# Kernel optimization log

Hardware: AMD Instinct MI355X
Metric: run time of the kernel (lower is better)

The kernel has to match this reference:

```python
import jax, jax.numpy as jnp
import numpy as np

LAMDA = 0.2  # config['lamda']
T, B, NI, IL, NS, H = 24, 64, 32, 24, 256, 256  # steps, batch, n_inputs, input_len(=vec), n_stations, hidden


def setup_inputs() -> dict:
    key = jax.random.key(0)
    ks = jax.random.split(key, 24)
    VEC, DIN = IL, NI + NS
    n = lambda k, s, sc=1.0: jax.random.normal(k, s, dtype=jnp.float32) * sc
    return {
        'local_inputs': n(ks[0], (T, B, NI)),
        'global_inputs': n(ks[1], (T, B, NS)),
        'local_states': n(ks[2], (B, NI, IL)),
        'global_states': n(ks[3], (B, NS, NI, IL)),
        'distmat': n(ks[4], (B, NS)),
        'local_attn0': jax.random.uniform(ks[5], (B, NI), jnp.float32, -0.25, 0.25),
        'global_attn0': jax.random.uniform(ks[6], (B, NS), jnp.float32, -0.15, 0.15),
        # conv_local_u: 1x1 conv over [B, IL, NI, 1] -> weight [VEC, IL]
        'Wcl': n(ks[7], (VEC, IL), 0.1), 'bcl': n(ks[8], (VEC,), 0.05),
        'Wll': n(ks[9], (VEC, H), 0.05), 'bll': n(ks[10], (VEC,), 0.05),
        'vl': n(ks[11], (VEC,)),
        # conv_global_k: kernel (1, NI) over [B, IL, NS, NI] -> weight [VEC, IL, NI]
        'Wcg': n(ks[12], (VEC, IL, NI), 0.05), 'bcg': n(ks[13], (VEC,), 0.05),
        'Wlg': n(ks[14], (VEC, H), 0.05), 'blg': n(ks[15], (VEC,), 0.05),
        'vg': n(ks[16], (VEC,)),
        # LSTM cell (called with zero h0/c0 every step, as in the source)
        'Wih': n(ks[17], (4 * H, DIN), 0.05),
        'bih': n(ks[18], (4 * H,), 0.05),
        'bhh': n(ks[19], (4 * H,), 0.05),
    }


def reference(local_inputs, global_inputs, local_states, global_states, distmat,
              local_attn0, global_attn0, Wcl, bcl, Wll, bll, vl,
              Wcg, bcg, Wlg, blg, vg, Wih, bih, bhh):
    b, ni, il = local_states.shape
    ns = global_states.shape[1]
    # raw .view() reshapes as in the torch code (NOT transposes)
    lhid = local_states.reshape(b, il, ni)                 # [B, IL, NI]
    hf_l = jnp.einsum('oc,bcl->bol', Wcl, lhid) + bcl[None, :, None]   # 1x1 conv
    ghid = global_states.reshape(b, il, ns, ni)            # [B, IL, NS, NI]
    hf_g = jnp.einsum('ocj,bcsj->bos', Wcg, ghid) + bcg[None, :, None]  # (1,NI) conv

    def step(carry, xs):
        la, ga = carry
        l_inp, g_inp = xs
        x = jnp.concatenate([la * l_inp, ga * g_inp], axis=1)  # [B, NI+NS]
        gates = x @ Wih.T + bih + bhh                          # h0 = 0 -> no Whh term
        i_g, f_g, g_g, o_g = jnp.split(gates, 4, axis=1)       # torch gate order i,f,g,o
        c = jax.nn.sigmoid(i_g) * jnp.tanh(g_g)                # c0 = 0 -> forget term drops
        h = jax.nn.sigmoid(o_g) * jnp.tanh(c)
        q = c                                                  # query = LSTM state
        y_l = q @ Wll.T + bll                                  # [B, VEC]
        s_l = jnp.einsum('bold,d->bl', jnp.tanh(hf_l[:, :, :, None] + y_l[:, None, None, :]), vl)
        la_n = jax.nn.softmax(s_l, axis=1)
        y_g = q @ Wlg.T + blg
        s_g = jnp.einsum('bosd,d->bs', jnp.tanh(hf_g[:, :, :, None] + y_g[:, None, None, :]), vg)
        s_g = (1.0 - LAMDA) * s_g + LAMDA * distmat
        ga_n = jax.nn.softmax(s_g, axis=1)
        return (la_n, ga_n), (h, c, la_n, ga_n)

    _, (outs, cs, las, gas) = jax.lax.scan(step, (local_attn0, global_attn0),
                                           (local_inputs, global_inputs))
    return outs, cs[-1], las, gas
```

## Files before the change

kernel.cpp:

```cpp
#include <hip/hip_runtime.h>

#define T_     24
#define LAMDA_ 0.2f

#define OFF_CS  393216
#define OFF_LAS 409600
#define OFF_GAS 458752

__device__ __forceinline__ float clamp15(float x){ return fminf(15.f, fmaxf(-15.f, x)); }
__device__ __forceinline__ float rcp_(float x){ return __builtin_amdgcn_rcpf(x); }

typedef float v2f __attribute__((ext_vector_type(2)));
typedef float v4f __attribute__((ext_vector_type(4)));
#define PKFMA(a,b,c) __builtin_elementwise_fma((a),(b),(c))

__global__ __launch_bounds__(1024, 4) void spat_kernel(
    const float* __restrict__ li,  const float* __restrict__ gi,
    const float* __restrict__ ls,  const float* __restrict__ gs,
    const float* __restrict__ dist,
    const float* __restrict__ la0, const float* __restrict__ ga0,
    const float* __restrict__ Wcl, const float* __restrict__ bcl,
    const float* __restrict__ Wll, const float* __restrict__ bll, const float* __restrict__ vl,
    const float* __restrict__ Wcg, const float* __restrict__ bcg,
    const float* __restrict__ Wlg, const float* __restrict__ blg, const float* __restrict__ vg,
    const float* __restrict__ Wih, const float* __restrict__ bih, const float* __restrict__ bhh,
    float* __restrict__ out)
{
    __shared__ float Eg[6144];
    __shared__ float El[800];
    __shared__ float outb[6144];
    __shared__ float gasb[6144];
    __shared__ float lasb[768];
    __shared__ float csb[256];
    __shared__ float slred[800];
    __shared__ __align__(16) union {
        float wcg[6144];
        struct {
            float sgred[1024];
            float xv[288];
            float cq[256];
            float slg[32];
        } p;
    } U;
    __shared__ float dstf[256];
    __shared__ float bsum[768];
    __shared__ float bcf[48];
    __shared__ __align__(16) float4 pl4[12], pg4[12];
    __shared__ float vlf[24], vgf[24], cbuf[2];

    const int b = blockIdx.x, tid = threadIdx.x;
    const int s = tid & 255, ogrp = tid >> 8;

    if (tid < 256) dstf[tid] = dist[b*256 + tid];
    if (tid < 24)  { vlf[tid] = vl[tid]; vgf[tid] = vg[tid]; }
    if (tid < 48)  bcf[tid] = (tid < 24) ? bll[tid] : blg[tid - 24];
    if (tid < 768) {
        const int wrow = tid + ((tid >= 256) ? 256 : 0);
        bsum[tid] = bih[wrow] + bhh[wrow];
    }
    if (tid == 0)  { float s1 = 0.f; for (int d = 0; d < 24; d++) s1 += vl[d]; cbuf[0] = s1; }
    if (tid == 1)  { float s1 = 0.f; for (int d = 0; d < 24; d++) s1 += vg[d]; cbuf[1] = s1; }

    v2f acc2[6];
#pragma unroll
    for (int i = 0; i < 6; i++) acc2[i] = (v2f){bcg[ogrp*6 + i], 0.f};

#pragma unroll 1
    for (int hc = 0; hc < 3; hc++) {
        for (int k = tid; k < 6144; k += 1024) {
            const int o = k >> 8, r = k & 255;
            U.wcg[k] = Wcg[o*768 + hc*256 + r];
        }
        __syncthreads();
#pragma unroll 1
        for (int cc = 0; cc < 8; cc++) {
            const int c = hc*8 + cc;
            const v4f* gp = (const v4f*)(gs + ((size_t)b*196608 + c*8192 + s*32));
#pragma unroll
            for (int h = 0; h < 2; h++) {
                const v4f g0 = gp[h*4 + 0], g1 = gp[h*4 + 1];
                const v4f g2 = gp[h*4 + 2], g3 = gp[h*4 + 3];
#pragma unroll
                for (int i = 0; i < 6; i++) {
                    const v4f* wp = (const v4f*)(U.wcg + ((ogrp*6 + i)*256 + cc*32)) + h*4;
                    const v4f w0 = wp[0], w1 = wp[1], w2 = wp[2], w3 = wp[3];
                    v2f a = acc2[i];
                    a = PKFMA(w0.xy, g0.xy, a); a = PKFMA(w0.zw, g0.zw, a);
                    a = PKFMA(w1.xy, g1.xy, a); a = PKFMA(w1.zw, g1.zw, a);
                    a = PKFMA(w2.xy, g2.xy, a); a = PKFMA(w2.zw, g2.zw, a);
                    a = PKFMA(w3.xy, g3.xy, a); a = PKFMA(w3.zw, g3.zw, a);
                    acc2[i] = a;
                }
            }
        }
        __syncthreads();
    }
#pragma unroll
    for (int i = 0; i < 6; i++)
        Eg[(ogrp*6 + i)*256 + s] = __expf(2.f*clamp15(acc2[i].x + acc2[i].y));

    if (tid < 768) {
        const int o = tid >> 5, l = tid & 31;
        float a = bcl[o];
        for (int c = 0; c < 24; c++)
            a = fmaf(Wcl[o*24 + c], ls[b*768 + c*32 + l], a);
        El[l*25 + o] = __expf(2.f*clamp15(a));
    }

    if (tid < 288) {
        if (tid < 32) U.p.xv[tid] = la0[b*32 + tid] * li[b*32 + tid];
        else { const int ss = tid - 32; U.p.xv[tid] = ga0[b*256 + ss] * gi[b*256 + ss]; }
    }
    __syncthreads();

    const int u8 = tid & 7, slot = tid >> 3;
    const int u0 = slot*2;

#pragma unroll 1
    for (int t = 0; t < T_; t++) {
        float liN = 0.f;
        float giN0 = 0.f, giN1 = 0.f, giN2 = 0.f, giN3 = 0.f;
        if (t < T_ - 1) {
            if (tid < 32) liN = li[(t+1)*2048 + b*32 + tid];
            else if (tid >= 64 && tid < 128) {
                const int lane = tid - 64;
                giN0 = gi[(t+1)*16384 + b*256 + lane];
                giN1 = gi[(t+1)*16384 + b*256 + lane + 64];
                giN2 = gi[(t+1)*16384 + b*256 + lane + 128];
                giN3 = gi[(t+1)*16384 + b*256 + lane + 192];
            }
        }

        {
            const v4f* xp = (const v4f*)U.p.xv;
            v2f br0 = {0.f,0.f}, br1 = {0.f,0.f}, br2 = {0.f,0.f};
            v2f br3 = {0.f,0.f}, br4 = {0.f,0.f}, br5 = {0.f,0.f};
#pragma unroll 1
            for (int jc = 0; jc < 3; jc++) {
                const v4f x0 = xp[jc*24 + u8];
                const v4f x1 = xp[jc*24 + 8 + u8];
                const v4f x2 = xp[jc*24 + 16 + u8];

#define KROW(WROW, AR) { \
                const v4f* wp_ = (const v4f*)(Wih + (size_t)(WROW)*288) + jc*24 + u8; \
                const v4f w0_ = wp_[0], w1_ = wp_[8], w2_ = wp_[16]; \
                v2f a_ = AR; \
                a_ = PKFMA(w0_.xy, x0.xy, a_); a_ = PKFMA(w0_.zw, x0.zw, a_); \
                a_ = PKFMA(w1_.xy, x1.xy, a_); a_ = PKFMA(w1_.zw, x1.zw, a_); \
                a_ = PKFMA(w2_.xy, x2.xy, a_); a_ = PKFMA(w2_.zw, x2.zw, a_); \
                AR = a_; }

                KROW(u0,       br0) KROW(512 + u0, br1) KROW(768 + u0, br2)
                __builtin_amdgcn_sched_barrier(0);
                KROW(u0 + 1,   br3) KROW(513 + u0, br4) KROW(769 + u0, br5)
                __builtin_amdgcn_sched_barrier(0);
#undef KROW
            }
            float ar0 = br0.x + br0.y, ar1 = br1.x + br1.y, ar2 = br2.x + br2.y;
            float ar3 = br3.x + br3.y, ar4 = br4.x + br4.y, ar5 = br5.x + br5.y;
            ar0 += __shfl_xor(ar0, 1); ar0 += __shfl_xor(ar0, 2); ar0 += __shfl_xor(ar0, 4);
            ar1 += __shfl_xor(ar1, 1); ar1 += __shfl_xor(ar1, 2); ar1 += __shfl_xor(ar1, 4);
            ar2 += __shfl_xor(ar2, 1); ar2 += __shfl_xor(ar2, 2); ar2 += __shfl_xor(ar2, 4);
            ar3 += __shfl_xor(ar3, 1); ar3 += __shfl_xor(ar3, 2); ar3 += __shfl_xor(ar3, 4);
            ar4 += __shfl_xor(ar4, 1); ar4 += __shfl_xor(ar4, 2); ar4 += __shfl_xor(ar4, 4);
            ar5 += __shfl_xor(ar5, 1); ar5 += __shfl_xor(ar5, 2); ar5 += __shfl_xor(ar5, 4);
            if (u8 < 2) {
                const int uu = u0 + u8;
                const float ig = (u8 ? ar3 : ar0) + bsum[uu];
                const float gg = (u8 ? ar4 : ar1) + bsum[256 + uu];
                const float ot = (u8 ? ar5 : ar2) + bsum[512 + uu];
                const float sig_i = rcp_(1.f + __expf(-ig));
                const float th_g  = 1.f - 2.f*rcp_(1.f + __expf(2.f*clamp15(gg)));
                const float c     = sig_i * th_g;
                const float sig_o = rcp_(1.f + __expf(-ot));
                const float th_c  = 1.f - 2.f*rcp_(1.f + __expf(2.f*c));
                const float h     = sig_o * th_c;
                U.p.cq[uu] = c;
                outb[t*256 + uu] = h;
                if (t == T_ - 1) csb[uu] = c;
            }
        }
        __syncthreads();

        if (tid < 768) {
            const int dot = tid >> 4, l16 = tid & 15;
            const float* Wr = (dot < 24) ? (Wll + dot*256) : (Wlg + (dot - 24)*256);
            const v4f* wp = (const v4f*)Wr + l16*4;
            const v4f* cp = (const v4f*)U.p.cq + l16*4;
            v2f a2 = {0.f, 0.f};
#pragma unroll
            for (int m = 0; m < 4; m++) {
                const v4f w0 = wp[m], c0 = cp[m];
                a2 = PKFMA(w0.xy, c0.xy, a2);
                a2 = PKFMA(w0.zw, c0.zw, a2);
            }
            float a = a2.x + a2.y;
            a += __shfl_xor(a, 1); a += __shfl_xor(a, 2);
            a += __shfl_xor(a, 4); a += __shfl_xor(a, 8);
            const float F  = __expf(2.f*clamp15(a + bcf[dot]));
            const float v  = (dot < 24) ? vlf[dot] : vgf[dot - 24];
            const float Fo = __shfl_xor(F, 16);
            const float vo = (dot < 24) ? vlf[dot ^ 1] : vgf[(dot ^ 1) - 24];
            if ((tid & 31) == 0) {
                const float A0 = v + vo;
                const float A1 = fmaf(v, Fo, vo * F);
                const float B1 = F + Fo;
                const float B2 = F * Fo;
                const int P2 = dot >> 1;
                if (P2 < 12) pl4[P2]      = make_float4(A0, A1, B1, B2);
                else         pg4[P2 - 12] = make_float4(A0, A1, B1, B2);
            }
        }
        __syncthreads();

        {
            float z[6];
#pragma unroll
            for (int i = 0; i < 6; i++) z[i] = Eg[(ogrp*6 + i)*256 + s];
            const v2f zv0 = {z[0], z[1]}, zv1 = {z[2], z[3]}, zv2 = {z[4], z[5]};
            const v2f z2v0 = zv0*zv0, z2v1 = zv1*zv1, z2v2 = zv2*zv2;
            const v2f one2 = {1.f, 1.f};
            v2f acc2d = {0.f, 0.f};
#pragma unroll 4
            for (int p = 0; p < 12; p++) {
                const float4 q = pg4[p];
                const v2f qx = {q.x, q.x}, qy = {q.y, q.y};
                const v2f qz = {q.z, q.z}, qw = {q.w, q.w};
                const v2f n0 = PKFMA(zv0, qy, qx);
                const v2f n1 = PKFMA(zv1, qy, qx);
                const v2f n2 = PKFMA(zv2, qy, qx);
                const v2f d0 = PKFMA(z2v0, qw, PKFMA(zv0, qz, one2));
                const v2f d1 = PKFMA(z2v1, qw, PKFMA(zv1, qz, one2));
                const v2f d2 = PKFMA(z2v2, qw, PKFMA(zv2, qz, one2));
                const v2f r0 = {rcp_(d0.x), rcp_(d0.y)};
                const v2f r1 = {rcp_(d1.x), rcp_(d1.y)};
                const v2f r2 = {rcp_(d2.x), rcp_(d2.y)};
                acc2d = PKFMA(n0, r0, acc2d);
                acc2d = PKFMA(n1, r1, acc2d);
                acc2d = PKFMA(n2, r2, acc2d);
            }
            U.p.sgred[tid] = acc2d.x + acc2d.y;
        }
        if (tid < 768) {
            const int l = tid / 24, o = tid - l*24;
            const float E  = El[l*25 + o];
            const float E2 = E*E;
            float b0 = 0.f, b1 = 0.f;
#pragma unroll 4
            for (int p = 0; p < 12; p += 2) {
                const float4 q0 = pl4[p], q1 = pl4[p+1];
                const float n0 = fmaf(E, q0.y, q0.x);
                const float d0 = fmaf(E2, q0.w, fmaf(E, q0.z, 1.f));
                const float n1 = fmaf(E, q1.y, q1.x);
                const float d1 = fmaf(E2, q1.w, fmaf(E, q1.z, 1.f));
                b0 = fmaf(n0, rcp_(d0), b0);
                b1 = fmaf(n1, rcp_(d1), b1);
            }
            slred[l*25 + o] = b0 + b1;
        }
        __syncthreads();

        if (tid < 32) {
            float tot = 0.f;
#pragma unroll
            for (int o2 = 0; o2 < 24; o2++) tot += slred[tid*25 + o2];
            const float sv = 24.f*cbuf[0] - 2.f*tot;
            float m = sv;
#pragma unroll
            for (int mk = 16; mk >= 1; mk >>= 1) m = fmaxf(m, __shfl_xor(m, mk));
            const float e = __expf(sv - m);
            float ss = e;
#pragma unroll
            for (int mk = 16; mk >= 1; mk >>= 1) ss += __shfl_xor(ss, mk);
            const float r = e * rcp_(ss);
            lasb[t*32 + tid] = r;
            if (t < T_ - 1) U.p.xv[tid] = r * liN;
        } else if (tid >= 64 && tid < 128) {
            const int lane = tid - 64;
            float vv0, vv1, vv2, vv3;
            {
                const float t0 = U.p.sgred[lane]     + U.p.sgred[256+lane]     + U.p.sgred[512+lane]     + U.p.sgred[768+lane];
                const float t1 = U.p.sgred[lane+64]  + U.p.sgred[256+lane+64]  + U.p.sgred[512+lane+64]  + U.p.sgred[768+lane+64];
                const float t2 = U.p.sgred[lane+128] + U.p.sgred[256+lane+128] + U.p.sgred[512+lane+128] + U.p.sgred[768+lane+128];
                const float t3 = U.p.sgred[lane+192] + U.p.sgred[256+lane+192] + U.p.sgred[512+lane+192] + U.p.sgred[768+lane+192];
                vv0 = (1.f-LAMDA_)*(24.f*cbuf[1] - 2.f*t0) + LAMDA_*dstf[lane];
                vv1 = (1.f-LAMDA_)*(24.f*cbuf[1] - 2.f*t1) + LAMDA_*dstf[lane+64];
                vv2 = (1.f-LAMDA_)*(24.f*cbuf[1] - 2.f*t2) + LAMDA_*dstf[lane+128];
                vv3 = (1.f-LAMDA_)*(24.f*cbuf[1] - 2.f*t3) + LAMDA_*dstf[lane+192];
            }
            float m = fmaxf(fmaxf(vv0, vv1), fmaxf(vv2, vv3));
#pragma unroll
            for (int mk = 32; mk >= 1; mk >>= 1) m = fmaxf(m, __shfl_xor(m, mk));
            const float e0 = __expf(vv0 - m), e1 = __expf(vv1 - m);
            const float e2 = __expf(vv2 - m), e3 = __expf(vv3 - m);
            float ss = (e0 + e1) + (e2 + e3);
#pragma unroll
            for (int mk = 32; mk >= 1; mk >>= 1) ss += __shfl_xor(ss, mk);
            const float inv = rcp_(ss);
            const float r0 = e0*inv, r1 = e1*inv, r2 = e2*inv, r3 = e3*inv;
            float* gb = gasb + t*256;
            gb[lane] = r0; gb[lane+64] = r1; gb[lane+128] = r2; gb[lane+192] = r3;
            if (t < T_ - 1) {
                U.p.xv[32+lane]     = r0 * giN0;
                U.p.xv[32+lane+64]  = r1 * giN1;
                U.p.xv[32+lane+128] = r2 * giN2;
                U.p.xv[32+lane+192] = r3 * giN3;
            }
        }
        __syncthreads();
    }

    for (int k = tid; k < 6144; k += 1024) {
        const int tt = k >> 8, ii = k & 255;
        out[tt*16384 + b*256 + ii]           = outb[k];
        out[OFF_GAS + tt*16384 + b*256 + ii] = gasb[k];
    }
    if (tid < 768) out[OFF_LAS + (tid >> 5)*2048 + b*32 + (tid & 31)] = lasb[tid];
    if (tid < 256) out[OFF_CS + b*256 + tid] = csb[tid];
}

extern "C" void kernel_launch(void* const* d_in, const int* in_sizes, int n_in,
                              void* d_out, int out_size, void* d_ws, size_t ws_size,
                              hipStream_t stream)
{
    const float* li   = (const float*)d_in[0];
    const float* gi   = (const float*)d_in[1];
    const float* ls   = (const float*)d_in[2];
    const float* gs   = (const float*)d_in[3];
    const float* dist = (const float*)d_in[4];
    const float* la0  = (const float*)d_in[5];
    const float* ga0  = (const float*)d_in[6];
    const float* Wcl  = (const float*)d_in[7];
    const float* bcl  = (const float*)d_in[8];
    const float* Wll  = (const float*)d_in[9];
    const float* bll  = (const float*)d_in[10];
    const float* vl   = (const float*)d_in[11];
    const float* Wcg  = (const float*)d_in[12];
    const float* bcg  = (const float*)d_in[13];
    const float* Wlg  = (const float*)d_in[14];
    const float* blg  = (const float*)d_in[15];
    const float* vg   = (const float*)d_in[16];
    const float* Wih  = (const float*)d_in[17];
    const float* bih  = (const float*)d_in[18];
    const float* bhh  = (const float*)d_in[19];

    spat_kernel<<<64, 1024, 0, stream>>>(li, gi, ls, gs, dist, la0, ga0,
                                         Wcl, bcl, Wll, bll, vl,
                                         Wcg, bcg, Wlg, blg, vg,
                                         Wih, bih, bhh, (float*)d_out);
}
```

Measured before the change: 478.8 us.

## Keep attention operands in registers and compute softmax redundantly per wave

```diff
diff --git a/kernel.cpp b/kernel.cpp
--- a/kernel.cpp
+++ b/kernel.cpp
@@ -26,7 +26,6 @@
     const float* __restrict__ Wih, const float* __restrict__ bih, const float* __restrict__ bhh,
     float* __restrict__ out)
 {
-    __shared__ float Eg[6144];
     __shared__ float El[800];
     __shared__ float outb[6144];
     __shared__ float gasb[6144];
@@ -39,7 +38,6 @@
             float sgred[1024];
             float xv[288];
             float cq[256];
-            float slg[32];
         } p;
     } U;
     __shared__ float dstf[256];
@@ -50,6 +48,7 @@
 
     const int b = blockIdx.x, tid = threadIdx.x;
     const int s = tid & 255, ogrp = tid >> 8;
+    const int lane = tid & 63, wid = tid >> 6;
 
     if (tid < 256) dstf[tid] = dist[b*256 + tid];
     if (tid < 24)  { vlf[tid] = vl[tid]; vgf[tid] = vg[tid]; }
@@ -95,9 +94,10 @@
         }
         __syncthreads();
     }
+    float Ewr[6];
 #pragma unroll
     for (int i = 0; i < 6; i++)
-        Eg[(ogrp*6 + i)*256 + s] = __expf(2.f*clamp15(acc2[i].x + acc2[i].y));
+        Ewr[i] = __expf(2.f*clamp15(acc2[i].x + acc2[i].y));
 
     if (tid < 768) {
         const int o = tid >> 5, l = tid & 31;
@@ -116,21 +116,12 @@
     const int u8 = tid & 7, slot = tid >> 3;
     const int u0 = slot*2;
 
+    const int l24 = tid / 24, o24 = tid - l24*24;
+    const float Elr = (tid < 768) ? El[l24*25 + o24] : 0.f;
+    const float El2r = Elr * Elr;
+
 #pragma unroll 1
     for (int t = 0; t < T_; t++) {
-        float liN = 0.f;
-        float giN0 = 0.f, giN1 = 0.f, giN2 = 0.f, giN3 = 0.f;
-        if (t < T_ - 1) {
-            if (tid < 32) liN = li[(t+1)*2048 + b*32 + tid];
-            else if (tid >= 64 && tid < 128) {
-                const int lane = tid - 64;
-                giN0 = gi[(t+1)*16384 + b*256 + lane];
-                giN1 = gi[(t+1)*16384 + b*256 + lane + 64];
-                giN2 = gi[(t+1)*16384 + b*256 + lane + 128];
-                giN3 = gi[(t+1)*16384 + b*256 + lane + 192];
-            }
-        }
-
         {
             const v4f* xp = (const v4f*)U.p.xv;
             v2f br0 = {0.f,0.f}, br1 = {0.f,0.f}, br2 = {0.f,0.f};
@@ -213,11 +204,17 @@
         }
         __syncthreads();
 
+        float liN = 0.f, giN0 = 0.f, giN1 = 0.f, giN2 = 0.f, giN3 = 0.f;
+        if (t < T_ - 1) {
+            if (lane < 32) liN = li[(t+1)*2048 + b*32 + lane];
+            giN0 = gi[(t+1)*16384 + b*256 + lane];
+            giN1 = gi[(t+1)*16384 + b*256 + lane + 64];
+            giN2 = gi[(t+1)*16384 + b*256 + lane + 128];
+            giN3 = gi[(t+1)*16384 + b*256 + lane + 192];
+        }
+
         {
-            float z[6];
-#pragma unroll
-            for (int i = 0; i < 6; i++) z[i] = Eg[(ogrp*6 + i)*256 + s];
-            const v2f zv0 = {z[0], z[1]}, zv1 = {z[2], z[3]}, zv2 = {z[4], z[5]};
+            const v2f zv0 = {Ewr[0], Ewr[1]}, zv1 = {Ewr[2], Ewr[3]}, zv2 = {Ewr[4], Ewr[5]};
             const v2f z2v0 = zv0*zv0, z2v1 = zv1*zv1, z2v2 = zv2*zv2;
             const v2f one2 = {1.f, 1.f};
             v2f acc2d = {0.f, 0.f};
@@ -242,52 +239,30 @@
             U.p.sgred[tid] = acc2d.x + acc2d.y;
         }
         if (tid < 768) {
-            const int l = tid / 24, o = tid - l*24;
-            const float E  = El[l*25 + o];
-            const float E2 = E*E;
             float b0 = 0.f, b1 = 0.f;
 #pragma unroll 4
             for (int p = 0; p < 12; p += 2) {
                 const float4 q0 = pl4[p], q1 = pl4[p+1];
-                const float n0 = fmaf(E, q0.y, q0.x);
-                const float d0 = fmaf(E2, q0.w, fmaf(E, q0.z, 1.f));
-                const float n1 = fmaf(E, q1.y, q1.x);
-                const float d1 = fmaf(E2, q1.w, fmaf(E, q1.z, 1.f));
+                const float n0 = fmaf(Elr, q0.y, q0.x);
+                const float d0 = fmaf(El2r, q0.w, fmaf(Elr, q0.z, 1.f));
+                const float n1 = fmaf(Elr, q1.y, q1.x);
+                const float d1 = fmaf(El2r, q1.w, fmaf(Elr, q1.z, 1.f));
                 b0 = fmaf(n0, rcp_(d0), b0);
                 b1 = fmaf(n1, rcp_(d1), b1);
             }
-            slred[l*25 + o] = b0 + b1;
-        }
-        __syncthreads();
-
-        if (tid < 32) {
-            float tot = 0.f;
-#pragma unroll
-            for (int o2 = 0; o2 < 24; o2++) tot += slred[tid*25 + o2];
-            const float sv = 24.f*cbuf[0] - 2.f*tot;
-            float m = sv;
-#pragma unroll
-            for (int mk = 16; mk >= 1; mk >>= 1) m = fmaxf(m, __shfl_xor(m, mk));
-            const float e = __expf(sv - m);
-            float ss = e;
-#pragma unroll
-            for (int mk = 16; mk >= 1; mk >>= 1) ss += __shfl_xor(ss, mk);
-            const float r = e * rcp_(ss);
-            lasb[t*32 + tid] = r;
-            if (t < T_ - 1) U.p.xv[tid] = r * liN;
-        } else if (tid >= 64 && tid < 128) {
-            const int lane = tid - 64;
-            float vv0, vv1, vv2, vv3;
-            {
-                const float t0 = U.p.sgred[lane]     + U.p.sgred[256+lane]     + U.p.sgred[512+lane]     + U.p.sgred[768+lane];
-                const float t1 = U.p.sgred[lane+64]  + U.p.sgred[256+lane+64]  + U.p.sgred[512+lane+64]  + U.p.sgred[768+lane+64];
-                const float t2 = U.p.sgred[lane+128] + U.p.sgred[256+lane+128] + U.p.sgred[512+lane+128] + U.p.sgred[768+lane+128];
-                const float t3 = U.p.sgred[lane+192] + U.p.sgred[256+lane+192] + U.p.sgred[512+lane+192] + U.p.sgred[768+lane+192];
-                vv0 = (1.f-LAMDA_)*(24.f*cbuf[1] - 2.f*t0) + LAMDA_*dstf[lane];
-                vv1 = (1.f-LAMDA_)*(24.f*cbuf[1] - 2.f*t1) + LAMDA_*dstf[lane+64];
-                vv2 = (1.f-LAMDA_)*(24.f*cbuf[1] - 2.f*t2) + LAMDA_*dstf[lane+128];
-                vv3 = (1.f-LAMDA_)*(24.f*cbuf[1] - 2.f*t3) + LAMDA_*dstf[lane+192];
-            }
+            slred[l24*25 + o24] = b0 + b1;
+        }
+        __syncthreads();
+
+        {
+            const float t0 = U.p.sgred[lane]     + U.p.sgred[256+lane]     + U.p.sgred[512+lane]     + U.p.sgred[768+lane];
+            const float t1 = U.p.sgred[lane+64]  + U.p.sgred[256+lane+64]  + U.p.sgred[512+lane+64]  + U.p.sgred[768+lane+64];
+            const float t2 = U.p.sgred[lane+128] + U.p.sgred[256+lane+128] + U.p.sgred[512+lane+128] + U.p.sgred[768+lane+128];
+            const float t3 = U.p.sgred[lane+192] + U.p.sgred[256+lane+192] + U.p.sgred[512+lane+192] + U.p.sgred[768+lane+192];
+            const float vv0 = (1.f-LAMDA_)*(24.f*cbuf[1] - 2.f*t0) + LAMDA_*dstf[lane];
+            const float vv1 = (1.f-LAMDA_)*(24.f*cbuf[1] - 2.f*t1) + LAMDA_*dstf[lane+64];
+            const float vv2 = (1.f-LAMDA_)*(24.f*cbuf[1] - 2.f*t2) + LAMDA_*dstf[lane+128];
+            const float vv3 = (1.f-LAMDA_)*(24.f*cbuf[1] - 2.f*t3) + LAMDA_*dstf[lane+192];
             float m = fmaxf(fmaxf(vv0, vv1), fmaxf(vv2, vv3));
 #pragma unroll
             for (int mk = 32; mk >= 1; mk >>= 1) m = fmaxf(m, __shfl_xor(m, mk));
@@ -298,17 +273,35 @@
             for (int mk = 32; mk >= 1; mk >>= 1) ss += __shfl_xor(ss, mk);
             const float inv = rcp_(ss);
             const float r0 = e0*inv, r1 = e1*inv, r2 = e2*inv, r3 = e3*inv;
-            float* gb = gasb + t*256;
-            gb[lane] = r0; gb[lane+64] = r1; gb[lane+128] = r2; gb[lane+192] = r3;
+            if (wid == 0) {
+                float* gb = gasb + t*256;
+                gb[lane] = r0; gb[lane+64] = r1; gb[lane+128] = r2; gb[lane+192] = r3;
+            }
             if (t < T_ - 1) {
                 U.p.xv[32+lane]     = r0 * giN0;
                 U.p.xv[32+lane+64]  = r1 * giN1;
                 U.p.xv[32+lane+128] = r2 * giN2;
                 U.p.xv[32+lane+192] = r3 * giN3;
             }
-        }
-        __syncthreads();
-    }
+            if (lane < 32) {
+                float tot = 0.f;
+#pragma unroll
+                for (int o2 = 0; o2 < 24; o2++) tot += slred[lane*25 + o2];
+                const float sv = 24.f*cbuf[0] - 2.f*tot;
+                float ml = sv;
+#pragma unroll
+                for (int mk = 16; mk >= 1; mk >>= 1) ml = fmaxf(ml, __shfl_xor(ml, mk));
+                const float e = __expf(sv - ml);
+                float ssl = e;
+#pragma unroll
+                for (int mk = 16; mk >= 1; mk >>= 1) ssl += __shfl_xor(ssl, mk);
+                const float r = e * rcp_(ssl);
+                if (wid == 0) lasb[t*32 + lane] = r;
+                if (t < T_ - 1) U.p.xv[lane] = r * liN;
+            }
+        }
+    }
+    __syncthreads();
 
     for (int k = tid; k < 6144; k += 1024) {
         const int tt = k >> 8, ii = k & 255;
```

Result: slower. 492.7 us (+2.9%).
